# Performance work log

Measured on AMD Instinct MI355X. Metric: run time of the kernel, lower is better.

The kernel has to match this reference:

```python
import jax, jax.numpy as jnp
import numpy as np

B, N, CIN, H, OUT, L, K = 8, 512, 64, 64, 64, 256, 3
EPS = 1e-5


def setup_inputs() -> dict:
    key = jax.random.key(0)
    ks = jax.random.split(key, 12)
    def unif(k, shape, fan):
        s = 1.0 / np.sqrt(fan)
        return jax.random.uniform(k, shape, jnp.float32, -s, s)
    return {
        "x": jax.random.normal(ks[0], (B, N, CIN, L), jnp.float32),
        "adj": jax.random.uniform(ks[1], (B, N, N), jnp.float32),
        # temp_conv1: Conv1d(CIN->H, k=3)
        "w1": unif(ks[2], (H, CIN, K), CIN * K),
        "b1": unif(ks[3], (H,), CIN * K),
        # graph_conv: Linear-style (H,H) + bias, stdv=1/sqrt(out_features)
        "gw": unif(ks[4], (H, H), H),
        "gb": unif(ks[5], (H,), H),
        # temp_conv2: Conv1d(H->OUT, k=3)
        "w2": unif(ks[6], (OUT, H, K), H * K),
        "b2": unif(ks[7], (OUT,), H * K),
        # residual: Conv1d(CIN->OUT, k=1) == pointwise linear
        "wr": unif(ks[8], (OUT, CIN), CIN),
        "br": unif(ks[9], (OUT,), CIN),
        # BatchNorm2d(OUT) affine params
        "gamma": jnp.ones((OUT,), jnp.float32),
        "beta": jnp.zeros((OUT,), jnp.float32),
    }


def _conv1d(x, w, b, pad):
    # x: (B, N, C, L) -> flatten node dim into batch, NCH conv
    b_, n_, c, l = x.shape
    y = jax.lax.conv_general_dilated(
        x.reshape(b_ * n_, c, l), w, window_strides=(1,),
        padding=[(pad, pad)], dimension_numbers=("NCH", "OIH", "NCH"))
    y = y + b[None, :, None]
    return y.reshape(b_, n_, w.shape[0], l)


def reference(x, adj, w1, b1, gw, gb, w2, b2, wr, br, gamma, beta):
    pad = (K - 1) // 2
    # residual branch: 1x1 conv over channels
    residual = jnp.einsum("bncl,oc->bnol", x, wr) + br[None, None, :, None]
    # temporal conv 1
    out = _conv1d(x, w1, b1, pad)                      # (B,N,H,L)
    # graph conv over all timesteps at once (replaces per-t Python loop)
    xw = jnp.einsum("bnhl,hd->bndl", out, gw)          # (B,N,H,L)
    out = jnp.einsum("bnm,bmdl->bndl", adj, xw) + gb[None, None, :, None]
    # temporal conv 2
    out = _conv1d(out, w2, b2, pad)                    # (B,N,OUT,L)
    out = out + residual
    # BatchNorm2d over channel axis (training-mode batch stats, biased var)
    mean = jnp.mean(out, axis=(0, 1, 3), keepdims=True)
    var = jnp.mean(jnp.square(out - mean), axis=(0, 1, 3), keepdims=True)
    out = (out - mean) * jax.lax.rsqrt(var + EPS)
    out = out * gamma[None, None, :, None] + beta[None, None, :, None]
    return jax.nn.relu(out)
```

## Files before the change

### kernel.cpp

```cpp
#include <hip/hip_runtime.h>
#include <hip/hip_bf16.h>
#include <stdint.h>


typedef unsigned short u16;
typedef unsigned int   u32;
typedef __attribute__((ext_vector_type(8))) short           bf16x8;
typedef __attribute__((ext_vector_type(8))) unsigned short  u16x8;
typedef __attribute__((ext_vector_type(4))) unsigned short  u16x4;
typedef __attribute__((ext_vector_type(4))) float           f32x4;

__device__ __forceinline__ float bf2f(u16 v){
  union { u32 u; float f; } x; x.u = ((u32)v) << 16; return x.f;
}
__device__ __forceinline__ u16 f2bf(float f){
  __hip_bfloat16 h = __float2bfloat16(f);
  return *reinterpret_cast<u16*>(&h);
}
__device__ __forceinline__ u32 swz(int row, int cbyte){
  return (u32)(row * 128) + (u32)(cbyte ^ ((row & 7) << 4));
}

__device__ __forceinline__ void stage_Tf(const float* __restrict__ src, u16* dst, int t){
  const int c0 = (t & 31) * 2;
  const int l0 = (t >> 5) * 32;
  #pragma unroll
  for (int v = 0; v < 8; ++v){
    f32x4 a = *(const f32x4*)(src + (size_t)c0 * 256 + l0 + v * 4);
    f32x4 b = *(const f32x4*)(src + (size_t)(c0 + 1) * 256 + l0 + v * 4);
    #pragma unroll
    for (int e = 0; e < 4; ++e){
      u32 p = (u32)f2bf(a[e]) | ((u32)f2bf(b[e]) << 16);
      *(u32*)((char*)dst + swz(l0 + v * 4 + e, c0 * 2)) = p;
    }
  }
}
__device__ __forceinline__ void stage_Tb(const u16* __restrict__ src, u16* dst, int t){
  const int c0 = (t & 31) * 2;
  const int l0 = (t >> 5) * 32;
  #pragma unroll
  for (int v = 0; v < 4; ++v){
    u16x8 a = *(const u16x8*)(src + (size_t)c0 * 256 + l0 + v * 8);
    u16x8 b = *(const u16x8*)(src + (size_t)(c0 + 1) * 256 + l0 + v * 8);
    #pragma unroll
    for (int e = 0; e < 8; ++e){
      u32 p = (u32)a[e] | ((u32)b[e] << 16);
      *(u32*)((char*)dst + swz(l0 + v * 8 + e, c0 * 2)) = p;
    }
  }
}

__global__ __launch_bounds__(256) void k_prep(const float* __restrict__ w1, const float* __restrict__ b1,
    const float* __restrict__ gw, const float* __restrict__ w2, const float* __restrict__ wr,
    u16* __restrict__ w1g, float* __restrict__ b1g, u16* __restrict__ w2t, u16* __restrict__ wrt){
  const int gt = blockIdx.x * 256 + threadIdx.x, gs = gridDim.x * 256;
  for (int e = gt; e < 12288; e += gs){
    int tap = e >> 12, rem = e & 4095, o = rem >> 6, c = rem & 63;
    w2t[e] = f2bf(w2[(o * 64 + c) * 3 + tap]);
    float s = 0.f;
    for (int h = 0; h < 64; ++h)
      s += gw[h * 64 + o] * w1[(h * 64 + c) * 3 + tap];
    w1g[e] = f2bf(s);
  }
  for (int e = gt; e < 4096; e += gs) wrt[e] = f2bf(wr[e]);
  for (int d = gt; d < 64; d += gs){
    float s = 0.f;
    for (int h = 0; h < 64; ++h) s += b1[h] * gw[h * 64 + d];
    b1g[d] = s;
  }
}

__global__ __launch_bounds__(256) void k_p1(const float* __restrict__ x,
    const u16* __restrict__ w1g, const float* __restrict__ b1g,
    const u16* __restrict__ wrt, u16* __restrict__ outA, u16* __restrict__ outR){
  __shared__ u16 tile[16384];
  const int t = threadIdx.x;
  const size_t bn = (size_t)blockIdx.x + (size_t)blockIdx.y * 512;
  stage_Tf(x + bn * 16384, tile, t);
  __syncthreads();
  const int w = t >> 6, ln = t & 63, lq = ln >> 4, lr = ln & 15;
  const bf16x8 z8 = {};

  {
    f32x4 racc[4][4];
    #pragma unroll
    for (int i = 0; i < 4; ++i)
      #pragma unroll
      for (int j = 0; j < 4; ++j) racc[i][j] = (f32x4){0.f, 0.f, 0.f, 0.f};
    #pragma unroll
    for (int kk = 0; kk < 2; ++kk){
      bf16x8 A[4];
      #pragma unroll
      for (int fo = 0; fo < 4; ++fo)
        A[fo] = *(const bf16x8*)(wrt + (fo * 16 + lr) * 64 + kk * 32 + lq * 8);
      #pragma unroll
      for (int fc = 0; fc < 4; ++fc){
        int l = w * 64 + fc * 16 + lr;
        bf16x8 B = *(const bf16x8*)((char*)tile + swz(l, kk * 64 + lq * 16));
        #pragma unroll
        for (int fo = 0; fo < 4; ++fo)
          racc[fo][fc] = __builtin_amdgcn_mfma_f32_16x16x32_bf16(A[fo], B, racc[fo][fc], 0, 0, 0);
      }
    }
    u16* rp = outR + bn * 16384 + t * 64;
    #pragma unroll
    for (int v = 0; v < 8; ++v){
      u16x8 ov;
      const int fo = v >> 1;
      #pragma unroll
      for (int h = 0; h < 2; ++h){
        const int fc = (v & 1) * 2 + h;
        #pragma unroll
        for (int r2 = 0; r2 < 4; ++r2)
          ov[h * 4 + r2] = f2bf(racc[fo][fc][r2]);
      }
      *(u16x8*)(rp + v * 8) = ov;
    }
  }

  f32x4 acc[4][4];
  #pragma unroll
  for (int i = 0; i < 4; ++i)
    #pragma unroll
    for (int j = 0; j < 4; ++j) acc[i][j] = (f32x4){0.f, 0.f, 0.f, 0.f};
  #pragma unroll
  for (int tap = 0; tap < 3; ++tap){
    #pragma unroll
    for (int kk = 0; kk < 2; ++kk){
      bf16x8 A[4];
      #pragma unroll
      for (int fo = 0; fo < 4; ++fo)
        A[fo] = *(const bf16x8*)(w1g + tap * 4096 + (fo * 16 + lr) * 64 + kk * 32 + lq * 8);
      #pragma unroll
      for (int fc = 0; fc < 4; ++fc){
        int r = w * 64 + fc * 16 + lr + tap - 1;
        int rc = r < 0 ? 0 : (r > 255 ? 255 : r);
        bf16x8 B = *(const bf16x8*)((char*)tile + swz(rc, kk * 64 + lq * 16));
        if (r != rc) B = z8;
        #pragma unroll
        for (int fo = 0; fo < 4; ++fo)
          acc[fo][fc] = __builtin_amdgcn_mfma_f32_16x16x32_bf16(A[fo], B, acc[fo][fc], 0, 0, 0);
      }
    }
  }
  __syncthreads();
  #pragma unroll
  for (int fo = 0; fo < 4; ++fo){
    float bb[4];
    #pragma unroll
    for (int r2 = 0; r2 < 4; ++r2) bb[r2] = b1g[fo * 16 + lq * 4 + r2];
    #pragma unroll
    for (int fc = 0; fc < 4; ++fc){
      int l = w * 64 + fc * 16 + lr;
      #pragma unroll
      for (int r2 = 0; r2 < 4; ++r2){
        int d = fo * 16 + lq * 4 + r2;
        tile[d * 256 + (l ^ ((d & 7) * 8))] = f2bf(acc[fo][fc][r2] + bb[r2]);
      }
    }
  }
  __syncthreads();
  u16* op = outA + bn * 16384;
  #pragma unroll
  for (int v = 0; v < 8; ++v){
    int d = (t >> 5) + v * 8;
    int l0 = (t & 31) * 8;
    u16x8 val = *(const u16x8*)(tile + d * 256 + (l0 ^ ((d & 7) * 8)));
    *(u16x8*)(op + v * 2048 + t * 8) = val;
  }
}

__global__ __launch_bounds__(256) void k_p3(const u16* __restrict__ xw,
    const float* __restrict__ adj, const float* __restrict__ gbv, u16* __restrict__ outB){
  __shared__ u16 At[8192];
  __shared__ u16 Bt[8192];
  const int t = threadIdx.x;
  const int wg = ((blockIdx.x & 7) << 9) | ((int)blockIdx.x >> 3);
  const int jt = wg & 127, nt = (wg >> 7) & 3, b = wg >> 9;
  const float* adjb = adj + ((size_t)b * 512 + (size_t)nt * 128) * 512;
  const u16* Xb = xw + (size_t)b * 8388608 + (size_t)jt * 128;
  const int w = t >> 6, ln = t & 63, lq = ln >> 4, lr = ln & 15;
  const int wrow = w >> 1, wcol = w & 1;
  const int mpair = t & 31, jq = t >> 5;
  f32x4 acc[4][4];
  #pragma unroll
  for (int i = 0; i < 4; ++i)
    #pragma unroll
    for (int j = 0; j < 4; ++j) acc[i][j] = (f32x4){0.f, 0.f, 0.f, 0.f};

  f32x4 ra[8];
  u16x8 rb[4];
  auto LOADK = [&](int ks){
    #pragma unroll
    for (int it = 0; it < 8; ++it){
      int c = it * 256 + t;
      int row = c >> 4, mc = c & 15;
      ra[it] = *(const f32x4*)(adjb + (size_t)row * 512 + ks * 64 + mc * 4);
    }
    const u16* s0 = Xb + (size_t)(ks * 64 + mpair * 2) * 16384 + jq * 16;
    const u16* s1 = s0 + 16384;
    #pragma unroll
    for (int v2 = 0; v2 < 2; ++v2){
      rb[v2 * 2]     = *(const u16x8*)(s0 + v2 * 8);
      rb[v2 * 2 + 1] = *(const u16x8*)(s1 + v2 * 8);
    }
  };

  LOADK(0);
  for (int ks = 0; ks < 8; ++ks){
    #pragma unroll
    for (int it = 0; it < 8; ++it){
      int c = it * 256 + t;
      int row = c >> 4, mc = c & 15;
      u16x4 pk;
      #pragma unroll
      for (int e = 0; e < 4; ++e) pk[e] = f2bf(ra[it][e]);
      *(u16x4*)((char*)At + (u32)(row * 128) + (u32)((mc * 8) ^ ((row & 7) << 4))) = pk;
    }
    #pragma unroll
    for (int v2 = 0; v2 < 2; ++v2){
      #pragma unroll
      for (int e = 0; e < 8; ++e){
        u32 p = (u32)(u16)rb[v2 * 2][e] | ((u32)(u16)rb[v2 * 2 + 1][e] << 16);
        *(u32*)((char*)Bt + swz(jq * 16 + v2 * 8 + e, mpair * 4)) = p;
      }
    }
    __syncthreads();
    if (ks < 7) LOADK(ks + 1);
    #pragma unroll
    for (int kk = 0; kk < 2; ++kk){
      bf16x8 Af[4], Bf[4];
      #pragma unroll
      for (int f = 0; f < 4; ++f){
        int rA = wrow * 64 + f * 16 + lr;
        Af[f] = *(const bf16x8*)((char*)At + swz(rA, kk * 64 + lq * 16));
        int rB = wcol * 64 + f * 16 + lr;
        Bf[f] = *(const bf16x8*)((char*)Bt + swz(rB, kk * 64 + lq * 16));
      }
      #pragma unroll
      for (int fr = 0; fr < 4; ++fr)
        #pragma unroll
        for (int fc = 0; fc < 4; ++fc)
          acc[fr][fc] = __builtin_amdgcn_mfma_f32_16x16x32_bf16(Af[fr], Bf[fc], acc[fr][fc], 0, 0, 0);
    }
    __syncthreads();
  }
  const float gb = gbv[jt >> 1];
  u16* ob = outB + ((size_t)b * 512 + (size_t)nt * 128) * 16384 + (size_t)jt * 128;
  #pragma unroll
  for (int fr = 0; fr < 4; ++fr)
    #pragma unroll
    for (int fc = 0; fc < 4; ++fc)
      #pragma unroll
      for (int r2 = 0; r2 < 4; ++r2){
        int n_ = wrow * 64 + fr * 16 + lq * 4 + r2;
        int j_ = wcol * 64 + fc * 16 + lr;
        ob[(size_t)n_ * 16384 + j_] = f2bf(acc[fr][fc][r2] + gb);
      }
}

__global__ __launch_bounds__(256) void k_p4(const u16* __restrict__ g,
    const u16* __restrict__ resv, const u16* __restrict__ w2t,
    const float* __restrict__ b2v, const float* __restrict__ brv,
    u16* __restrict__ outP, float* __restrict__ spart){
  __shared__ u16 gt[16384];
  __shared__ float sc2[512];
  const int t = threadIdx.x;
  const size_t bn = (size_t)blockIdx.x + (size_t)blockIdx.y * 512;
  stage_Tb(g + bn * 16384, gt, t);
  __syncthreads();
  const int w = t >> 6, ln = t & 63, lq = ln >> 4, lr = ln & 15;
  const bf16x8 z8 = {};

  const u16* rp = resv + bn * 16384 + t * 64;
  u16x8 rv[8];
  #pragma unroll
  for (int v = 0; v < 8; ++v) rv[v] = *(const u16x8*)(rp + v * 8);

  f32x4 acc[4][4];
  #pragma unroll
  for (int i = 0; i < 4; ++i)
    #pragma unroll
    for (int j = 0; j < 4; ++j) acc[i][j] = (f32x4){0.f, 0.f, 0.f, 0.f};

  #pragma unroll
  for (int tap = 0; tap < 3; ++tap){
    #pragma unroll
    for (int kk = 0; kk < 2; ++kk){
      bf16x8 A[4];
      #pragma unroll
      for (int fo = 0; fo < 4; ++fo)
        A[fo] = *(const bf16x8*)(w2t + tap * 4096 + (fo * 16 + lr) * 64 + kk * 32 + lq * 8);
      #pragma unroll
      for (int fc = 0; fc < 4; ++fc){
        int r = w * 64 + fc * 16 + lr + tap - 1;
        int rc = r < 0 ? 0 : (r > 255 ? 255 : r);
        bf16x8 B = *(const bf16x8*)((char*)gt + swz(rc, kk * 64 + lq * 16));
        if (r != rc) B = z8;
        #pragma unroll
        for (int fo = 0; fo < 4; ++fo)
          acc[fo][fc] = __builtin_amdgcn_mfma_f32_16x16x32_bf16(A[fo], B, acc[fo][fc], 0, 0, 0);
      }
    }
  }
  __syncthreads();

  float psum[16], psq[16];
  #pragma unroll
  for (int i = 0; i < 16; ++i){ psum[i] = 0.f; psq[i] = 0.f; }
  #pragma unroll
  for (int fo = 0; fo < 4; ++fo){
    float bb[4];
    #pragma unroll
    for (int r2 = 0; r2 < 4; ++r2){
      int o = fo * 16 + lq * 4 + r2;
      bb[r2] = b2v[o] + brv[o];
    }
    #pragma unroll
    for (int fc = 0; fc < 4; ++fc){
      int l = w * 64 + fc * 16 + lr;
      #pragma unroll
      for (int r2 = 0; r2 < 4; ++r2){
        float val = acc[fo][fc][r2] + bb[r2]
                  + bf2f(rv[fo * 2 + (fc >> 1)][(fc & 1) * 4 + r2]);
        int d = fo * 16 + lq * 4 + r2;
        gt[d * 256 + (l ^ ((d & 7) * 8))] = f2bf(val);
        psum[fo * 4 + r2] += val;
        psq[fo * 4 + r2] += val * val;
      }
    }
  }
  #pragma unroll
  for (int i = 0; i < 16; ++i){
    #pragma unroll
    for (int m = 1; m < 16; m <<= 1){
      psum[i] += __shfl_xor(psum[i], m, 64);
      psq[i]  += __shfl_xor(psq[i],  m, 64);
    }
  }
  if (lr == 0){
    #pragma unroll
    for (int i = 0; i < 16; ++i){
      int o = (i >> 2) * 16 + lq * 4 + (i & 3);
      sc2[w * 128 + o]      = psum[i];
      sc2[w * 128 + 64 + o] = psq[i];
    }
  }
  __syncthreads();
  u16* op = outP + bn * 16384;
  #pragma unroll
  for (int v = 0; v < 8; ++v){
    int d = (t >> 5) + v * 8;
    int l0 = (t & 31) * 8;
    u16x8 val = *(const u16x8*)(gt + d * 256 + (l0 ^ ((d & 7) * 8)));
    *(u16x8*)(op + v * 2048 + t * 8) = val;
  }
  if (t < 128){
    float tot = sc2[t] + sc2[128 + t] + sc2[256 + t] + sc2[384 + t];
    spart[(size_t)t * 4096 + bn] = tot;
  }
}

__global__ __launch_bounds__(256) void k_p5(const float* __restrict__ part, float* __restrict__ fin){
  const int o = blockIdx.x, t = threadIdx.x;
  float s1 = 0.f, s2 = 0.f;
  for (int k = t; k < 4096; k += 256){
    s1 += part[(size_t)o * 4096 + k];
    s2 += part[(size_t)(64 + o) * 4096 + k];
  }
  #pragma unroll
  for (int m = 32; m; m >>= 1){
    s1 += __shfl_down(s1, m, 64);
    s2 += __shfl_down(s2, m, 64);
  }
  __shared__ float red[8];
  if ((t & 63) == 0){ red[(t >> 6) * 2] = s1; red[(t >> 6) * 2 + 1] = s2; }
  __syncthreads();
  if (t == 0){
    float S1 = red[0] + red[2] + red[4] + red[6];
    float S2 = red[1] + red[3] + red[5] + red[7];
    const float invN = 1.f / 1048576.f;
    float mean = S1 * invN;
    float var = S2 * invN - mean * mean;
    fin[o] = mean;
    fin[64 + o] = rsqrtf(var + 1e-5f);
  }
}

__global__ __launch_bounds__(256) void k_p6(const u16* __restrict__ pre, const float* __restrict__ fin,
    const float* __restrict__ gamma, const float* __restrict__ beta, float* __restrict__ out){
  __shared__ float ssca[64], soff[64];
  const int tt = threadIdx.x;
  if (tt < 64){
    float sc = fin[64 + tt] * gamma[tt];
    ssca[tt] = sc;
    soff[tt] = beta[tt] - fin[tt] * sc;
  }
  __syncthreads();
  const size_t nchunk = 8388608;
  for (size_t i = (size_t)blockIdx.x * 256 + tt; i < nchunk; i += (size_t)gridDim.x * 256){
    int o = (int)((i >> 5) & 63);
    float sca = ssca[o], off = soff[o];
    u16x8 v = *(const u16x8*)(pre + i * 8);
    f32x4 oa, ob;
    #pragma unroll
    for (int e = 0; e < 4; ++e){
      float f0 = bf2f(v[e]) * sca + off;
      float f1 = bf2f(v[4 + e]) * sca + off;
      oa[e] = f0 > 0.f ? f0 : 0.f;
      ob[e] = f1 > 0.f ? f1 : 0.f;
    }
    *(f32x4*)(out + i * 8)     = oa;
    *(f32x4*)(out + i * 8 + 4) = ob;
  }
}

extern "C" void kernel_launch(void* const* d_in, const int* in_sizes, int n_in,
                              void* d_out, int out_size, void* d_ws, size_t ws_size,
                              hipStream_t stream){
  const float* x     = (const float*)d_in[0];
  const float* adj   = (const float*)d_in[1];
  const float* w1    = (const float*)d_in[2];
  const float* b1    = (const float*)d_in[3];
  const float* gw    = (const float*)d_in[4];
  const float* gb    = (const float*)d_in[5];
  const float* w2    = (const float*)d_in[6];
  const float* b2    = (const float*)d_in[7];
  const float* wr    = (const float*)d_in[8];
  const float* br    = (const float*)d_in[9];
  const float* gamma = (const float*)d_in[10];
  const float* beta  = (const float*)d_in[11];
  (void)in_sizes; (void)n_in; (void)out_size; (void)ws_size;

  char* ws = (char*)d_ws;
  u16*   bufA  = (u16*)ws;
  float* spart = (float*)(ws + 134217728);
  float* sfin  = (float*)(ws + 136314880);
  u16*   w1g   = (u16*)(ws + 136315392);
  float* b1g   = (float*)(ws + 136339968);
  u16*   w2t   = (u16*)(ws + 136348160);
  u16*   wrt   = (u16*)(ws + 136372736);
  u16*   gbuf  = (u16*)d_out;
  u16*   bufR  = (u16*)d_out + 67108864;

  k_prep<<<16, 256, 0, stream>>>(w1, b1, gw, w2, wr, w1g, b1g, w2t, wrt);
  k_p1<<<dim3(512, 8, 1), 256, 0, stream>>>(x, w1g, b1g, wrt, bufA, bufR);
  k_p3<<<4096, 256, 0, stream>>>(bufA, adj, gb, gbuf);
  k_p4<<<dim3(512, 8, 1), 256, 0, stream>>>(gbuf, bufR, w2t, b2, br, bufA, spart);
  k_p5<<<64, 256, 0, stream>>>(spart, sfin);
  k_p6<<<2048, 256, 0, stream>>>(bufA, sfin, gamma, beta, (float*)d_out);
}
```

Before: 558.9 us.

## Store intermediate activations time-major so graph and conv2 stages load contiguously

The first-stage kernel now writes its bf16 output as (L, channel) per node instead of (channel, L), and the graph-conv kernel treats columns as (l, d) pairs with a per-column bias. The conv2 kernel can then stage its input with plain contiguous 16-byte copies into the swizzled tile instead of a transposing gather. The x staging loop is also re-indexed for more coalesced reads. The aim is to cut scattered global and LDS traffic in the staging phases. The cost is that the intermediate layout must agree across three kernels.

New measurement: 553.2 us. No clear change (-1.0%).

```diff
diff --git a/kernel.cpp b/kernel.cpp
--- a/kernel.cpp
+++ b/kernel.cpp
@@ -19,35 +19,6 @@
 }
 __device__ __forceinline__ u32 swz(int row, int cbyte){
   return (u32)(row * 128) + (u32)(cbyte ^ ((row & 7) << 4));
-}
-
-__device__ __forceinline__ void stage_Tf(const float* __restrict__ src, u16* dst, int t){
-  const int c0 = (t & 31) * 2;
-  const int l0 = (t >> 5) * 32;
-  #pragma unroll
-  for (int v = 0; v < 8; ++v){
-    f32x4 a = *(const f32x4*)(src + (size_t)c0 * 256 + l0 + v * 4);
-    f32x4 b = *(const f32x4*)(src + (size_t)(c0 + 1) * 256 + l0 + v * 4);
-    #pragma unroll
-    for (int e = 0; e < 4; ++e){
-      u32 p = (u32)f2bf(a[e]) | ((u32)f2bf(b[e]) << 16);
-      *(u32*)((char*)dst + swz(l0 + v * 4 + e, c0 * 2)) = p;
-    }
-  }
-}
-__device__ __forceinline__ void stage_Tb(const u16* __restrict__ src, u16* dst, int t){
-  const int c0 = (t & 31) * 2;
-  const int l0 = (t >> 5) * 32;
-  #pragma unroll
-  for (int v = 0; v < 4; ++v){
-    u16x8 a = *(const u16x8*)(src + (size_t)c0 * 256 + l0 + v * 8);
-    u16x8 b = *(const u16x8*)(src + (size_t)(c0 + 1) * 256 + l0 + v * 8);
-    #pragma unroll
-    for (int e = 0; e < 8; ++e){
-      u32 p = (u32)a[e] | ((u32)b[e] << 16);
-      *(u32*)((char*)dst + swz(l0 + v * 8 + e, c0 * 2)) = p;
-    }
-  }
 }
 
 __global__ __launch_bounds__(256) void k_prep(const float* __restrict__ w1, const float* __restrict__ b1,
@@ -76,7 +47,22 @@
   __shared__ u16 tile[16384];
   const int t = threadIdx.x;
   const size_t bn = (size_t)blockIdx.x + (size_t)blockIdx.y * 512;
-  stage_Tf(x + bn * 16384, tile, t);
+  const float* xb = x + bn * 16384;
+
+  {
+    const int c0 = (t >> 3) * 2;
+    #pragma unroll
+    for (int v = 0; v < 8; ++v){
+      const int l0 = (t & 7) * 4 + v * 32;
+      f32x4 a = *(const f32x4*)(xb + (size_t)c0 * 256 + l0);
+      f32x4 b = *(const f32x4*)(xb + (size_t)(c0 + 1) * 256 + l0);
+      #pragma unroll
+      for (int e = 0; e < 4; ++e){
+        u32 p = (u32)f2bf(a[e]) | ((u32)f2bf(b[e]) << 16);
+        *(u32*)((char*)tile + swz(l0 + e, c0 * 2)) = p;
+      }
+    }
+  }
   __syncthreads();
   const int w = t >> 6, ln = t & 63, lq = ln >> 4, lr = ln & 15;
   const bf16x8 z8 = {};
@@ -155,7 +141,7 @@
       #pragma unroll
       for (int r2 = 0; r2 < 4; ++r2){
         int d = fo * 16 + lq * 4 + r2;
-        tile[d * 256 + (l ^ ((d & 7) * 8))] = f2bf(acc[fo][fc][r2] + bb[r2]);
+        *(u16*)((char*)tile + l * 128 + ((2 * d) ^ ((l & 7) << 4))) = f2bf(acc[fo][fc][r2] + bb[r2]);
       }
     }
   }
@@ -163,10 +149,10 @@
   u16* op = outA + bn * 16384;
   #pragma unroll
   for (int v = 0; v < 8; ++v){
-    int d = (t >> 5) + v * 8;
-    int l0 = (t & 31) * 8;
-    u16x8 val = *(const u16x8*)(tile + d * 256 + (l0 ^ ((d & 7) * 8)));
-    *(u16x8*)(op + v * 2048 + t * 8) = val;
+    int flat = v * 2048 + t * 8;
+    int l = flat >> 6, d0 = flat & 63;
+    u16x8 val = *(const u16x8*)((char*)tile + l * 128 + ((d0 * 2) ^ ((l & 7) << 4)));
+    *(u16x8*)(op + flat) = val;
   }
 }
 
@@ -245,7 +231,9 @@
     }
     __syncthreads();
   }
-  const float gb = gbv[jt >> 1];
+  float gbl[4];
+  #pragma unroll
+  for (int fc = 0; fc < 4; ++fc) gbl[fc] = gbv[fc * 16 + lr];
   u16* ob = outB + ((size_t)b * 512 + (size_t)nt * 128) * 16384 + (size_t)jt * 128;
   #pragma unroll
   for (int fr = 0; fr < 4; ++fr)
@@ -255,7 +243,7 @@
       for (int r2 = 0; r2 < 4; ++r2){
         int n_ = wrow * 64 + fr * 16 + lq * 4 + r2;
         int j_ = wcol * 64 + fc * 16 + lr;
-        ob[(size_t)n_ * 16384 + j_] = f2bf(acc[fr][fc][r2] + gb);
+        ob[(size_t)n_ * 16384 + j_] = f2bf(acc[fr][fc][r2] + gbl[fc]);
       }
 }
 
@@ -263,11 +251,18 @@
     const u16* __restrict__ resv, const u16* __restrict__ w2t,
     const float* __restrict__ b2v, const float* __restrict__ brv,
     u16* __restrict__ outP, float* __restrict__ spart){
-  __shared__ u16 gt[16384];
+  __shared__ u16 gt2[16384];
   __shared__ float sc2[512];
   const int t = threadIdx.x;
   const size_t bn = (size_t)blockIdx.x + (size_t)blockIdx.y * 512;
-  stage_Tb(g + bn * 16384, gt, t);
+  const u16* gb = g + bn * 16384;
+  #pragma unroll
+  for (int v = 0; v < 8; ++v){
+    int flat = v * 2048 + t * 8;
+    int l = flat >> 6, d0 = flat & 63;
+    u16x8 val = *(const u16x8*)(gb + flat);
+    *(u16x8*)((char*)gt2 + l * 128 + ((d0 * 2) ^ ((l & 7) << 4))) = val;
+  }
   __syncthreads();
   const int w = t >> 6, ln = t & 63, lq = ln >> 4, lr = ln & 15;
   const bf16x8 z8 = {};
@@ -295,7 +290,7 @@
       for (int fc = 0; fc < 4; ++fc){
         int r = w * 64 + fc * 16 + lr + tap - 1;
         int rc = r < 0 ? 0 : (r > 255 ? 255 : r);
-        bf16x8 B = *(const bf16x8*)((char*)gt + swz(rc, kk * 64 + lq * 16));
+        bf16x8 B = *(const bf16x8*)((char*)gt2 + swz(rc, kk * 64 + lq * 16));
         if (r != rc) B = z8;
         #pragma unroll
         for (int fo = 0; fo < 4; ++fo)
@@ -323,8 +318,8 @@
       for (int r2 = 0; r2 < 4; ++r2){
         float val = acc[fo][fc][r2] + bb[r2]
                   + bf2f(rv[fo * 2 + (fc >> 1)][(fc & 1) * 4 + r2]);
-        int d = fo * 16 + lq * 4 + r2;
-        gt[d * 256 + (l ^ ((d & 7) * 8))] = f2bf(val);
+        int o = fo * 16 + lq * 4 + r2;
+        gt2[o * 256 + (l ^ ((o & 7) * 8))] = f2bf(val);
         psum[fo * 4 + r2] += val;
         psq[fo * 4 + r2] += val * val;
       }
@@ -352,7 +347,7 @@
   for (int v = 0; v < 8; ++v){
     int d = (t >> 5) + v * 8;
     int l0 = (t & 31) * 8;
-    u16x8 val = *(const u16x8*)(gt + d * 256 + (l0 ^ ((d & 7) * 8)));
+    u16x8 val = *(const u16x8*)(gt2 + d * 256 + (l0 ^ ((d & 7) * 8)));
     *(u16x8*)(op + v * 2048 + t * 8) = val;
   }
   if (t < 128){
```
